# Kernel tuning notes

Hardware: AMD Instinct MI355X
Metric: run time of the kernel (lower is better)

Reference implementation:

```python
import jax, jax.numpy as jnp
import numpy as np

T, B, E, H = 2048, 2, 2048, 16
HD = E // H
SCALE = HD ** -0.5
NEG = -1e9  # large-negative additive mask (finite, safe in fp32/bf16)


def setup_inputs() -> dict:
    key = jax.random.key(0)
    ks = jax.random.split(key, 6)
    query = jax.random.normal(ks[0], (T, B, E), dtype=jnp.float32)
    # causal additive mask, as metaseq builds for decoder self-attention
    attn_mask = jnp.where(jnp.tril(jnp.ones((T, T), dtype=bool)), 0.0, NEG).astype(jnp.float32)
    # combined qkv projection: rows ordered [K | V | Q] per split_tensor_along_last_dim
    qkv_w = jax.random.normal(ks[1], (3 * E, E), dtype=jnp.float32) * (1.0 / np.sqrt(2 * E))
    qkv_b = jax.random.uniform(ks[2], (3 * E,), dtype=jnp.float32, minval=-1, maxval=1) / np.sqrt(E)
    out_w = jax.random.normal(ks[3], (E, E), dtype=jnp.float32) * (1.0 / np.sqrt(2 * E))
    out_b = jax.random.uniform(ks[4], (E,), dtype=jnp.float32, minval=-1, maxval=1) / np.sqrt(E)
    return {"query": query, "attn_mask": attn_mask, "qkv_w": qkv_w,
            "qkv_b": qkv_b, "out_w": out_w, "out_b": out_b}


def reference(query, attn_mask, qkv_w, qkv_b, out_w, out_b):
    t, b, e = query.shape
    # fused QKV projection (ColumnParallelLinear, world_size=1)
    kvq = jnp.einsum('tbe,fe->tbf', query, qkv_w) + qkv_b  # [T,B,3E]
    k, v, q = kvq[..., :e], kvq[..., e:2 * e], kvq[..., 2 * e:]
    q = q * SCALE
    q = q.reshape(t, b, H, HD)
    k = k.reshape(t, b, H, HD)
    v = v.reshape(t, b, H, HD)
    # explicit QK^T bmm -> [B,H,T,S]
    scores = jnp.einsum('tbhd,sbhd->bhts', q, k) + attn_mask[None, None]
    probs = jax.nn.softmax(scores, axis=-1)  # dropout p=0 -> identity
    ctx = jnp.einsum('bhts,sbhd->tbhd', probs, v).reshape(t, b, e)
    # RowParallelLinear out_proj (skip_bias_add in the original; bias added here)
    out = jnp.einsum('tbe,fe->tbf', ctx, out_w) + out_b
    return out
```

## Files before the change

### kernel.cpp

```cpp
#include <hip/hip_runtime.h>
#include <hip/hip_bf16.h>
#include <stdint.h>

#define T_DIM 2048
#define B_DIM 2
#define E_DIM 2048
#define H_DIM 16
#define HD_DIM 128
#define F_DIM 6144
#define ROWS 4096
#define KVB 64

#define QK_SCALE 0.08838834764831845f
#define LOG2E    1.4426950408889634f
#define RESCALE_THR 8.0f

typedef __bf16 bf16_t;
typedef __bf16 bf16x8 __attribute__((ext_vector_type(8)));
typedef __bf16 bf16x4 __attribute__((ext_vector_type(4)));
typedef float  f32x4  __attribute__((ext_vector_type(4)));

__device__ __forceinline__ void gll16(const void* g, void* l) {
  __builtin_amdgcn_global_load_lds((const __attribute__((address_space(1))) void*)g,
                                   (__attribute__((address_space(3))) void*)l, 16, 0, 0);
}

__global__ void cvt_f32_bf16(const float* __restrict__ src, bf16_t* __restrict__ dst, int n4) {
  int i = blockIdx.x * blockDim.x + threadIdx.x;
  int stride = gridDim.x * blockDim.x;
  for (; i < n4; i += stride) {
    float4 v = ((const float4*)src)[i];
    bf16x4 o;
    o[0] = (bf16_t)v.x; o[1] = (bf16_t)v.y; o[2] = (bf16_t)v.z; o[3] = (bf16_t)v.w;
    ((bf16x4*)dst)[i] = o;
  }
}

template<int EPI>
__launch_bounds__(256, 2)
__global__ void gemm_bt(const bf16_t* __restrict__ A, const bf16_t* __restrict__ Bm,
                        const float* __restrict__ bias, void* __restrict__ Cout,
                        int N, int K, int nbn, float qscale, int qcol0)
{
  __shared__ __align__(16) bf16_t As[128][64];
  __shared__ __align__(16) bf16_t Bs[128][64];

  int bid = blockIdx.x;
  int nwg = gridDim.x;
  int cpx = nwg >> 3;
  int swz = (bid & 7) * cpx + (bid >> 3);
  int bm = swz / nbn, bn = swz % nbn;

  int tid = threadIdx.x;
  int lane = tid & 63, wid = tid >> 6;
  int lr = lane & 15, lg = lane >> 4;
  int wm = wid >> 1, wn = wid & 1;

  f32x4 acc[4][4] = {};

  int srow8 = tid >> 3;
  int schunk = tid & 7;

  const bf16_t* gA = A + (size_t)(bm * 128) * K;
  const bf16_t* gB = Bm + (size_t)(bn * 128) * K;

  for (int k0 = 0; k0 < K; k0 += 64) {
    #pragma unroll
    for (int i = 0; i < 4; ++i) {
      int row = i * 32 + srow8;
      int sc = schunk ^ (row & 7);
      gll16(gA + (size_t)row * K + k0 + sc * 8, &As[row][schunk * 8]);
    }
    #pragma unroll
    for (int i = 0; i < 4; ++i) {
      int row = i * 32 + srow8;
      int sc = schunk ^ (row & 7);
      gll16(gB + (size_t)row * K + k0 + sc * 8, &Bs[row][schunk * 8]);
    }
    __syncthreads();

    #pragma unroll
    for (int kk = 0; kk < 2; ++kk) {
      bf16x8 af[4], bfr[4];
      #pragma unroll
      for (int mi = 0; mi < 4; ++mi) {
        int row = wm * 64 + mi * 16 + lr;
        int ch = (kk * 4 + lg) ^ (row & 7);
        af[mi] = *(const bf16x8*)&As[row][ch * 8];
      }
      #pragma unroll
      for (int ni = 0; ni < 4; ++ni) {
        int row = wn * 64 + ni * 16 + lr;
        int ch = (kk * 4 + lg) ^ (row & 7);
        bfr[ni] = *(const bf16x8*)&Bs[row][ch * 8];
      }
      #pragma unroll
      for (int mi = 0; mi < 4; ++mi)
        #pragma unroll
        for (int ni = 0; ni < 4; ++ni)
          acc[mi][ni] = __builtin_amdgcn_mfma_f32_16x16x32_bf16(af[mi], bfr[ni], acc[mi][ni], 0, 0, 0);
    }
    __syncthreads();
  }

  #pragma unroll
  for (int mi = 0; mi < 4; ++mi) {
    int row0 = bm * 128 + wm * 64 + mi * 16 + lg * 4;
    #pragma unroll
    for (int ni = 0; ni < 4; ++ni) {
      int col = bn * 128 + wn * 64 + ni * 16 + lr;
      float bv = bias[col];
      float scl = (EPI == 0 && col >= qcol0) ? qscale : 1.0f;
      #pragma unroll
      for (int r = 0; r < 4; ++r) {
        float v = (acc[mi][ni][r] + bv) * scl;
        if (EPI == 0) ((bf16_t*)Cout)[(size_t)(row0 + r) * N + col] = (bf16_t)v;
        else          ((float*)Cout)[(size_t)(row0 + r) * N + col] = v;
      }
    }
  }
}

__global__ void repack_vt(const bf16_t* __restrict__ KVQ, bf16_t* __restrict__ VTg)
{
  __shared__ __align__(16) bf16_t tile[64][136];
  int bid = blockIdx.x;
  int st = bid & 31, bh = bid >> 5;
  int b = bh >> 4, h = bh & 15;
  int s0 = st * 64;
  int tid = threadIdx.x;

  const bf16_t* vbase = KVQ + (size_t)b * F_DIM + E_DIM + (size_t)h * HD_DIM;
  #pragma unroll
  for (int i = 0; i < 4; ++i) {
    int row = i * 16 + (tid >> 4), c = tid & 15;
    bf16x8 v = *(const bf16x8*)(vbase + (size_t)(s0 + row) * B_DIM * F_DIM + c * 8);
    *(bf16x8*)&tile[row][c * 8] = v;
  }
  __syncthreads();
  bf16_t* out = VTg + (size_t)bh * HD_DIM * T_DIM;
  #pragma unroll
  for (int i = 0; i < 4; ++i) {
    int d = i * 32 + (tid >> 3), c = tid & 7;
    bf16x8 o;
    #pragma unroll
    for (int j = 0; j < 8; ++j) o[j] = tile[c * 8 + j][d];
    *(bf16x8*)(out + (size_t)d * T_DIM + s0 + c * 8) = o;
  }
}

__launch_bounds__(256, 2)
__global__ void attn3(const bf16_t* __restrict__ KVQ, const bf16_t* __restrict__ VTg,
                      bf16_t* __restrict__ CTX)
{
  __shared__ __align__(16) bf16_t Ks[2][KVB][128];
  __shared__ __align__(16) bf16_t Vs[2][128][KVB];
  __shared__ __align__(16) bf16_t Ps[4][32 * 64];

  int bid = blockIdx.x;
  int xcd = bid & 7;
  int j   = bid >> 3;
  int hi  = j >> 5;
  int mid = (j >> 4) & 1;
  int q   = j & 15;
  int bh  = xcd * 4 + hi * 2 + mid;
  int qt  = hi ? (15 - q) : q;
  int b = bh >> 4, h = bh & 15;

  int tid = threadIdx.x;
  int lane = tid & 63, wid = tid >> 6;
  int lr = lane & 15, lg = lane >> 4;

  const bf16_t* kbase = KVQ + (size_t)b * F_DIM + (size_t)h * HD_DIM;
  const bf16_t* vtb   = VTg + (size_t)bh * HD_DIM * T_DIM;
  bf16_t* PsW = &Ps[wid][0];

  bf16x8 qf[2][4];
  #pragma unroll
  for (int mf = 0; mf < 2; ++mf) {
    int t = qt * 128 + wid * 32 + mf * 16 + lr;
    const bf16_t* qb = KVQ + ((size_t)t * B_DIM + b) * F_DIM + 2 * E_DIM + h * HD_DIM;
    #pragma unroll
    for (int ks = 0; ks < 4; ++ks) qf[mf][ks] = *(const bf16x8*)(qb + ks * 32 + lg * 8);
  }

  f32x4 ctxa[2][8] = {};
  float m[2][4], lsum[2][4];
  #pragma unroll
  for (int mf = 0; mf < 2; ++mf)
    #pragma unroll
    for (int r = 0; r < 4; ++r) { m[mf][r] = -1e30f; lsum[mf][r] = 0.0f; }

  int krow = tid >> 4, kch = tid & 15;
  int vrow = tid >> 3, vch = tid & 7;

  auto stage = [&](int buf, int it) {
    int s0 = it * KVB;
    #pragma unroll
    for (int i = 0; i < 4; ++i) {
      int row = i * 16 + krow;
      int sc = kch ^ (row & 7);
      gll16(kbase + (size_t)(s0 + row) * B_DIM * F_DIM + sc * 8, &Ks[buf][row][kch * 8]);
    }
    #pragma unroll
    for (int i = 0; i < 4; ++i) {
      int row = i * 32 + vrow;
      int sc = vch ^ (row & 7);
      gll16(vtb + (size_t)row * T_DIM + s0 + sc * 8, &Vs[buf][row][vch * 8]);
    }
  };

  int nt = 2 * (qt + 1);
  stage(0, 0);
  __syncthreads();

  int tqw = qt * 128 + wid * 32;

  for (int it = 0; it < nt; ++it) {
    int cur = it & 1;
    if (it + 1 < nt) stage(cur ^ 1, it + 1);
    int s0 = it * KVB;
    bool diag = (it >= nt - 2);

    f32x4 sacc[2][4] = {};
    __builtin_amdgcn_s_setprio(1);
    #pragma unroll
    for (int ks = 0; ks < 4; ++ks) {
      #pragma unroll
      for (int nti = 0; nti < 4; ++nti) {
        int srow = nti * 16 + lr;
        int slot = (ks * 4 + lg) ^ (srow & 7);
        bf16x8 kf = *(const bf16x8*)&Ks[cur][srow][slot * 8];
        sacc[0][nti] = __builtin_amdgcn_mfma_f32_16x16x32_bf16(qf[0][ks], kf, sacc[0][nti], 0, 0, 0);
        sacc[1][nti] = __builtin_amdgcn_mfma_f32_16x16x32_bf16(qf[1][ks], kf, sacc[1][nti], 0, 0, 0);
      }
    }
    __builtin_amdgcn_s_setprio(0);

    float mxl = -1e30f;
    #pragma unroll
    for (int mf = 0; mf < 2; ++mf)
      #pragma unroll
      for (int r = 0; r < 4; ++r)
        #pragma unroll
        for (int nti = 0; nti < 4; ++nti) {
          float v = sacc[mf][nti][r];
          if (diag) v = (s0 + nti * 16 + lr > tqw + mf * 16 + lg * 4 + r) ? -1e30f : v;
          sacc[mf][nti][r] = v;
          mxl = fmaxf(mxl, v - m[mf][r]);
        }
    if (!__all(mxl <= RESCALE_THR)) {
      #pragma unroll
      for (int mf = 0; mf < 2; ++mf)
        #pragma unroll
        for (int r = 0; r < 4; ++r) {
          float mx = fmaxf(fmaxf(sacc[mf][0][r], sacc[mf][1][r]),
                           fmaxf(sacc[mf][2][r], sacc[mf][3][r]));
          #pragma unroll
          for (int d = 1; d < 16; d <<= 1) mx = fmaxf(mx, __shfl_xor(mx, d, 64));
          float mn = fmaxf(m[mf][r], mx);
          float rs = exp2f(m[mf][r] - mn);
          m[mf][r] = mn;
          lsum[mf][r] *= rs;
          #pragma unroll
          for (int dt = 0; dt < 8; ++dt) ctxa[mf][dt][r] *= rs;
        }
    }
    #pragma unroll
    for (int mf = 0; mf < 2; ++mf)
      #pragma unroll
      for (int r = 0; r < 4; ++r) {
        int prow = mf * 16 + lg * 4 + r;
        #pragma unroll
        for (int nti = 0; nti < 4; ++nti) {
          float p = exp2f(sacc[mf][nti][r] - m[mf][r]);
          lsum[mf][r] += p;
          int chk = (nti * 2 + (lr >> 3)) ^ (prow & 7);
          PsW[prow * 64 + chk * 8 + (lr & 7)] = (bf16_t)p;
        }
      }
    asm volatile("s_waitcnt lgkmcnt(0)" ::: "memory");
    __builtin_amdgcn_sched_barrier(0);

    bf16x8 pf[2][2];
    #pragma unroll
    for (int mf = 0; mf < 2; ++mf) {
      int prow = mf * 16 + lr;
      #pragma unroll
      for (int kh = 0; kh < 2; ++kh) {
        int chk = (kh * 4 + lg) ^ (prow & 7);
        pf[mf][kh] = *(const bf16x8*)&PsW[prow * 64 + chk * 8];
      }
    }
    __builtin_amdgcn_s_setprio(1);
    #pragma unroll
    for (int dt = 0; dt < 8; ++dt) {
      int drow = dt * 16 + lr;
      int sl0 = lg ^ (drow & 7);
      int sl1 = (4 + lg) ^ (drow & 7);
      bf16x8 vf0 = *(const bf16x8*)&Vs[cur][drow][sl0 * 8];
      bf16x8 vf1 = *(const bf16x8*)&Vs[cur][drow][sl1 * 8];
      ctxa[0][dt] = __builtin_amdgcn_mfma_f32_16x16x32_bf16(pf[0][0], vf0, ctxa[0][dt], 0, 0, 0);
      ctxa[0][dt] = __builtin_amdgcn_mfma_f32_16x16x32_bf16(pf[0][1], vf1, ctxa[0][dt], 0, 0, 0);
      ctxa[1][dt] = __builtin_amdgcn_mfma_f32_16x16x32_bf16(pf[1][0], vf0, ctxa[1][dt], 0, 0, 0);
      ctxa[1][dt] = __builtin_amdgcn_mfma_f32_16x16x32_bf16(pf[1][1], vf1, ctxa[1][dt], 0, 0, 0);
    }
    __builtin_amdgcn_s_setprio(0);

    __syncthreads();
  }

  #pragma unroll
  for (int mf = 0; mf < 2; ++mf)
    #pragma unroll
    for (int r = 0; r < 4; ++r) {
      #pragma unroll
      for (int d = 1; d < 16; d <<= 1) lsum[mf][r] += __shfl_xor(lsum[mf][r], d, 64);
    }

  #pragma unroll
  for (int mf = 0; mf < 2; ++mf)
    #pragma unroll
    for (int r = 0; r < 4; ++r) {
      int t = qt * 128 + wid * 32 + mf * 16 + lg * 4 + r;
      float inv = 1.0f / lsum[mf][r];
      bf16_t* out = CTX + ((size_t)t * B_DIM + b) * E_DIM + h * HD_DIM;
      #pragma unroll
      for (int dt = 0; dt < 8; ++dt)
        out[dt * 16 + lr] = (bf16_t)(ctxa[mf][dt][r] * inv);
    }
}

extern "C" void kernel_launch(void* const* d_in, const int* in_sizes, int n_in,
                              void* d_out, int out_size, void* d_ws, size_t ws_size,
                              hipStream_t stream)
{
  const float* query = (const float*)d_in[0];
  const float* qkv_w = (const float*)d_in[2];
  const float* qkv_b = (const float*)d_in[3];
  const float* out_w = (const float*)d_in[4];
  const float* out_b = (const float*)d_in[5];

  bf16_t* Xbf  = (bf16_t*)d_ws;
  bf16_t* Wqkv = Xbf  + (size_t)ROWS * E_DIM;
  bf16_t* Wout = Wqkv + (size_t)F_DIM * E_DIM;
  bf16_t* KVQ  = Wout + (size_t)E_DIM * E_DIM;
  bf16_t* CTX  = Xbf;
  bf16_t* VTg  = Wqkv;

  cvt_f32_bf16<<<2048, 256, 0, stream>>>(query, Xbf,  ROWS * E_DIM / 4);
  cvt_f32_bf16<<<2048, 256, 0, stream>>>(qkv_w, Wqkv, F_DIM * E_DIM / 4);
  cvt_f32_bf16<<<2048, 256, 0, stream>>>(out_w, Wout, E_DIM * E_DIM / 4);

  gemm_bt<0><<<32 * 48, 256, 0, stream>>>(Xbf, Wqkv, qkv_b, KVQ,
                                          F_DIM, E_DIM, 48, QK_SCALE * LOG2E, 2 * E_DIM);

  repack_vt<<<32 * 32, 256, 0, stream>>>(KVQ, VTg);

  attn3<<<512, 256, 0, stream>>>(KVQ, VTg, CTX);

  gemm_bt<1><<<32 * 16, 256, 0, stream>>>(CTX, Wout, out_b, (float*)d_out,
                                          E_DIM, E_DIM, 16, 1.0f, 1 << 30);
}
```

Before: 281.7 us.

## Triple-buffer GEMM LDS loads with 128x256 tiles and 512-thread blocks

Replaces the single-buffered 128x128 GEMM with a 512-thread kernel that computes 128x256 tiles and prefetches two K-steps ahead into a three-slot LDS ring using direct global-to-LDS loads. Explicit vmcnt waits and raw barriers replace the per-step syncthreads. All fragments are preloaded before the MFMA burst, which runs at raised wave priority. The aim is to hide global load latency and raise operand reuse. The cost is much more LDS per block (~144KB), which may limit occupancy to one block per CU, plus fewer blocks for the output projection (256).

```diff
diff --git a/kernel.cpp b/kernel.cpp
--- a/kernel.cpp
+++ b/kernel.cpp
@@ -37,70 +37,96 @@
 }
 
 template<int EPI>
-__launch_bounds__(256, 2)
-__global__ void gemm_bt(const bf16_t* __restrict__ A, const bf16_t* __restrict__ Bm,
+__launch_bounds__(512, 2)
+__global__ void gemm_dp(const bf16_t* __restrict__ A, const bf16_t* __restrict__ Bm,
                         const float* __restrict__ bias, void* __restrict__ Cout,
                         int N, int K, int nbn, float qscale, int qcol0)
 {
-  __shared__ __align__(16) bf16_t As[128][64];
-  __shared__ __align__(16) bf16_t Bs[128][64];
+  __shared__ __align__(16) bf16_t As[3][128][64];
+  __shared__ __align__(16) bf16_t Bs[3][256][64];
 
   int bid = blockIdx.x;
-  int nwg = gridDim.x;
-  int cpx = nwg >> 3;
+  int cpx = gridDim.x >> 3;
   int swz = (bid & 7) * cpx + (bid >> 3);
   int bm = swz / nbn, bn = swz % nbn;
 
   int tid = threadIdx.x;
   int lane = tid & 63, wid = tid >> 6;
   int lr = lane & 15, lg = lane >> 4;
-  int wm = wid >> 1, wn = wid & 1;
+  int wm = wid >> 2, wn = wid & 3;
 
   f32x4 acc[4][4] = {};
 
-  int srow8 = tid >> 3;
+  int srow = tid >> 3;
   int schunk = tid & 7;
 
   const bf16_t* gA = A + (size_t)(bm * 128) * K;
-  const bf16_t* gB = Bm + (size_t)(bn * 128) * K;
-
-  for (int k0 = 0; k0 < K; k0 += 64) {
+  const bf16_t* gB = Bm + (size_t)(bn * 256) * K;
+
+  int nt = K >> 6;
+
+  auto stage = [&](int kt, int slot) {
+    int k0 = kt * 64;
+    #pragma unroll
+    for (int i = 0; i < 2; ++i) {
+      int row = i * 64 + srow;
+      int sc = schunk ^ (row & 7);
+      gll16(gA + (size_t)row * K + k0 + sc * 8, &As[slot][row][schunk * 8]);
+    }
     #pragma unroll
     for (int i = 0; i < 4; ++i) {
-      int row = i * 32 + srow8;
+      int row = i * 64 + srow;
       int sc = schunk ^ (row & 7);
-      gll16(gA + (size_t)row * K + k0 + sc * 8, &As[row][schunk * 8]);
-    }
-    #pragma unroll
-    for (int i = 0; i < 4; ++i) {
-      int row = i * 32 + srow8;
-      int sc = schunk ^ (row & 7);
-      gll16(gB + (size_t)row * K + k0 + sc * 8, &Bs[row][schunk * 8]);
-    }
-    __syncthreads();
-
+      gll16(gB + (size_t)row * K + k0 + sc * 8, &Bs[slot][row][schunk * 8]);
+    }
+  };
+
+  stage(0, 0);
+  if (nt > 1) stage(1, 1);
+
+  for (int t = 0; t < nt; ++t) {
+    int slot = t % 3;
+    if (t + 2 < nt) {
+      stage(t + 2, (t + 2) % 3);
+      asm volatile("s_waitcnt vmcnt(12)" ::: "memory");
+    } else if (t + 2 == nt) {
+      asm volatile("s_waitcnt vmcnt(6)" ::: "memory");
+    } else {
+      asm volatile("s_waitcnt vmcnt(0)" ::: "memory");
+    }
+    __builtin_amdgcn_sched_barrier(0);
+    __builtin_amdgcn_s_barrier();
+    __builtin_amdgcn_sched_barrier(0);
+
+    bf16x8 af[2][4], bfm[2][4];
     #pragma unroll
     for (int kk = 0; kk < 2; ++kk) {
-      bf16x8 af[4], bfr[4];
       #pragma unroll
       for (int mi = 0; mi < 4; ++mi) {
         int row = wm * 64 + mi * 16 + lr;
         int ch = (kk * 4 + lg) ^ (row & 7);
-        af[mi] = *(const bf16x8*)&As[row][ch * 8];
+        af[kk][mi] = *(const bf16x8*)&As[slot][row][ch * 8];
       }
       #pragma unroll
       for (int ni = 0; ni < 4; ++ni) {
         int row = wn * 64 + ni * 16 + lr;
         int ch = (kk * 4 + lg) ^ (row & 7);
-        bfr[ni] = *(const bf16x8*)&Bs[row][ch * 8];
-      }
+        bfm[kk][ni] = *(const bf16x8*)&Bs[slot][row][ch * 8];
+      }
+    }
+    __builtin_amdgcn_s_setprio(1);
+    #pragma unroll
+    for (int kk = 0; kk < 2; ++kk)
       #pragma unroll
       for (int mi = 0; mi < 4; ++mi)
         #pragma unroll
         for (int ni = 0; ni < 4; ++ni)
-          acc[mi][ni] = __builtin_amdgcn_mfma_f32_16x16x32_bf16(af[mi], bfr[ni], acc[mi][ni], 0, 0, 0);
-    }
-    __syncthreads();
+          acc[mi][ni] = __builtin_amdgcn_mfma_f32_16x16x32_bf16(af[kk][mi], bfm[kk][ni], acc[mi][ni], 0, 0, 0);
+    __builtin_amdgcn_s_setprio(0);
+
+    __builtin_amdgcn_sched_barrier(0);
+    __builtin_amdgcn_s_barrier();
+    __builtin_amdgcn_sched_barrier(0);
   }
 
   #pragma unroll
@@ -108,7 +134,7 @@
     int row0 = bm * 128 + wm * 64 + mi * 16 + lg * 4;
     #pragma unroll
     for (int ni = 0; ni < 4; ++ni) {
-      int col = bn * 128 + wn * 64 + ni * 16 + lr;
+      int col = bn * 256 + wn * 64 + ni * 16 + lr;
       float bv = bias[col];
       float scl = (EPI == 0 && col >= qcol0) ? qscale : 1.0f;
       #pragma unroll
@@ -352,13 +378,13 @@
   cvt_f32_bf16<<<2048, 256, 0, stream>>>(qkv_w, Wqkv, F_DIM * E_DIM / 4);
   cvt_f32_bf16<<<2048, 256, 0, stream>>>(out_w, Wout, E_DIM * E_DIM / 4);
 
-  gemm_bt<0><<<32 * 48, 256, 0, stream>>>(Xbf, Wqkv, qkv_b, KVQ,
-                                          F_DIM, E_DIM, 48, QK_SCALE * LOG2E, 2 * E_DIM);
+  gemm_dp<0><<<768, 512, 0, stream>>>(Xbf, Wqkv, qkv_b, KVQ,
+                                      F_DIM, E_DIM, 24, QK_SCALE * LOG2E, 2 * E_DIM);
 
   repack_vt<<<32 * 32, 256, 0, stream>>>(KVQ, VTg);
 
   attn3<<<512, 256, 0, stream>>>(KVQ, VTg, CTX);
 
-  gemm_bt<1><<<32 * 16, 256, 0, stream>>>(CTX, Wout, out_b, (float*)d_out,
-                                          E_DIM, E_DIM, 16, 1.0f, 1 << 30);
-}
+  gemm_dp<1><<<256, 512, 0, stream>>>(CTX, Wout, out_b, (float*)d_out,
+                                      E_DIM, E_DIM, 8, 1.0f, 1 << 30);
+}
```

Measured after the change: 308.3 us. 1.09x slower.

## Use 256x256-tile double-buffered GEMM with 8 waves for QKV projection

Applied to the files above, without the earlier changes.

Replaces the 128x128-tile QKV projection GEMM with a new 512-thread kernel that computes 256x256 output tiles. It double-buffers 64-wide K slices in LDS, loaded asynchronously with XOR swizzling, and splits each iteration's MFMA work into two halves so the next stage's loads start mid-iteration. Raising MFMA priority during compute aims to keep the matrix units busy. The larger tile improves data reuse and cuts global traffic, but it uses 128 KB of LDS per block and yields only 384 blocks, which may reduce occupancy and leave part of the GPU idle at the tail.

```diff
diff --git a/kernel.cpp b/kernel.cpp
--- a/kernel.cpp
+++ b/kernel.cpp
@@ -119,6 +119,134 @@
       }
     }
   }
+}
+
+template<int EPI>
+__launch_bounds__(512, 2)
+__global__ void gemm_dp2(const bf16_t* __restrict__ A, const bf16_t* __restrict__ Bm,
+                         const float* __restrict__ bias, void* __restrict__ Cout,
+                         int N, int K, int nbn, float qscale, int qcol0)
+{
+  __shared__ __align__(16) bf16_t As[2][256][64];
+  __shared__ __align__(16) bf16_t Bs[2][256][64];
+
+  int bid = blockIdx.x;
+  int cpx = gridDim.x >> 3;
+  int swz = (bid & 7) * cpx + (bid >> 3);
+  int bm = swz / nbn, bn = swz % nbn;
+
+  int tid = threadIdx.x;
+  int lane = tid & 63, wid = tid >> 6;
+  int lr = lane & 15, lg = lane >> 4;
+  int wm = wid >> 2, wn = wid & 3;
+
+  f32x4 acc[8][4] = {};
+
+  int srow = tid >> 3;
+  int schunk = tid & 7;
+
+  const bf16_t* gA = A + (size_t)(bm * 256) * K;
+  const bf16_t* gB = Bm + (size_t)(bn * 256) * K;
+
+  int nt = K >> 6;
+
+  auto stage = [&](int kt, int buf) {
+    int k0 = kt * 64;
+    #pragma unroll
+    for (int i = 0; i < 4; ++i) {
+      int row = i * 64 + srow;
+      int sc = schunk ^ (row & 7);
+      gll16(gA + (size_t)row * K + k0 + sc * 8, &As[buf][row][schunk * 8]);
+    }
+    #pragma unroll
+    for (int i = 0; i < 4; ++i) {
+      int row = i * 64 + srow;
+      int sc = schunk ^ (row & 7);
+      gll16(gB + (size_t)row * K + k0 + sc * 8, &Bs[buf][row][schunk * 8]);
+    }
+  };
+
+  stage(0, 0);
+  if (nt > 1) stage(1, 1);
+  asm volatile("s_waitcnt vmcnt(8)" ::: "memory");
+  asm volatile("s_barrier" ::: "memory");
+
+  for (int t = 0; t < nt; ++t) {
+    int buf = t & 1;
+
+    bf16x8 a0[4][2], bfr[4][2];
+    #pragma unroll
+    for (int mi = 0; mi < 4; ++mi)
+      #pragma unroll
+      for (int kk = 0; kk < 2; ++kk) {
+        int row = wm * 128 + mi * 16 + lr;
+        int ch = (kk * 4 + lg) ^ (row & 7);
+        a0[mi][kk] = *(const bf16x8*)&As[buf][row][ch * 8];
+      }
+    #pragma unroll
+    for (int ni = 0; ni < 4; ++ni)
+      #pragma unroll
+      for (int kk = 0; kk < 2; ++kk) {
+        int row = wn * 64 + ni * 16 + lr;
+        int ch = (kk * 4 + lg) ^ (row & 7);
+        bfr[ni][kk] = *(const bf16x8*)&Bs[buf][row][ch * 8];
+      }
+    __builtin_amdgcn_s_setprio(1);
+    #pragma unroll
+    for (int kk = 0; kk < 2; ++kk)
+      #pragma unroll
+      for (int mi = 0; mi < 4; ++mi)
+        #pragma unroll
+        for (int ni = 0; ni < 4; ++ni)
+          acc[mi][ni] = __builtin_amdgcn_mfma_f32_16x16x32_bf16(a0[mi][kk], bfr[ni][kk], acc[mi][ni], 0, 0, 0);
+    __builtin_amdgcn_s_setprio(0);
+
+    bf16x8 a1[4][2];
+    #pragma unroll
+    for (int mi = 0; mi < 4; ++mi)
+      #pragma unroll
+      for (int kk = 0; kk < 2; ++kk) {
+        int row = wm * 128 + 64 + mi * 16 + lr;
+        int ch = (kk * 4 + lg) ^ (row & 7);
+        a1[mi][kk] = *(const bf16x8*)&As[buf][row][ch * 8];
+      }
+    asm volatile("s_waitcnt lgkmcnt(0)" ::: "memory");
+    asm volatile("s_barrier" ::: "memory");
+    if (t + 2 < nt) stage(t + 2, buf);
+
+    __builtin_amdgcn_s_setprio(1);
+    #pragma unroll
+    for (int kk = 0; kk < 2; ++kk)
+      #pragma unroll
+      for (int mi = 0; mi < 4; ++mi)
+        #pragma unroll
+        for (int ni = 0; ni < 4; ++ni)
+          acc[4 + mi][ni] = __builtin_amdgcn_mfma_f32_16x16x32_bf16(a1[mi][kk], bfr[ni][kk], acc[4 + mi][ni], 0, 0, 0);
+    __builtin_amdgcn_s_setprio(0);
+
+    if (t + 2 < nt)      asm volatile("s_waitcnt vmcnt(8)" ::: "memory");
+    else if (t + 1 < nt) asm volatile("s_waitcnt vmcnt(0)" ::: "memory");
+    asm volatile("s_barrier" ::: "memory");
+  }
+
+  #pragma unroll
+  for (int qm = 0; qm < 2; ++qm)
+    #pragma unroll
+    for (int mi = 0; mi < 4; ++mi) {
+      int row0 = bm * 256 + wm * 128 + qm * 64 + mi * 16 + lg * 4;
+      #pragma unroll
+      for (int ni = 0; ni < 4; ++ni) {
+        int col = bn * 256 + wn * 64 + ni * 16 + lr;
+        float bv = bias[col];
+        float scl = (EPI == 0 && col >= qcol0) ? qscale : 1.0f;
+        #pragma unroll
+        for (int r = 0; r < 4; ++r) {
+          float v = (acc[qm * 4 + mi][ni][r] + bv) * scl;
+          if (EPI == 0) ((bf16_t*)Cout)[(size_t)(row0 + r) * N + col] = (bf16_t)v;
+          else          ((float*)Cout)[(size_t)(row0 + r) * N + col] = v;
+        }
+      }
+    }
 }
 
 __global__ void repack_vt(const bf16_t* __restrict__ KVQ, bf16_t* __restrict__ VTg)
@@ -352,8 +480,8 @@
   cvt_f32_bf16<<<2048, 256, 0, stream>>>(qkv_w, Wqkv, F_DIM * E_DIM / 4);
   cvt_f32_bf16<<<2048, 256, 0, stream>>>(out_w, Wout, E_DIM * E_DIM / 4);
 
-  gemm_bt<0><<<32 * 48, 256, 0, stream>>>(Xbf, Wqkv, qkv_b, KVQ,
-                                          F_DIM, E_DIM, 48, QK_SCALE * LOG2E, 2 * E_DIM);
+  gemm_dp2<0><<<384, 512, 0, stream>>>(Xbf, Wqkv, qkv_b, KVQ,
+                                       F_DIM, E_DIM, 24, QK_SCALE * LOG2E, 2 * E_DIM);
 
   repack_vt<<<32 * 32, 256, 0, stream>>>(KVQ, VTg);
 
```

Measured after the change: 272.5 us. 1.03x faster.

## Use 256x256-tile 8-wave ping-pong GEMM for QKV projection

Applied to the files above, without the earlier changes.

Adds a new GEMM kernel with 256x256 output tiles, 512 threads (8 waves), double-buffered LDS filled by direct global-to-LDS loads, and a four-phase schedule that interleaves quadrant MFMAs with prefetches under barriers and raised wave priority. It replaces the 128x128 QKV projection launch to raise arithmetic intensity and overlap loads with compute. The cost is a large LDS footprint (128KB), heavy register use, and only 384 blocks, which may limit occupancy and leave a wave-quantization tail. The out-projection still uses the old kernel.

```diff
diff --git a/kernel.cpp b/kernel.cpp
--- a/kernel.cpp
+++ b/kernel.cpp
@@ -119,6 +119,149 @@
       }
     }
   }
+}
+
+template<int EPI>
+__launch_bounds__(512, 2)
+__global__ void gemm_8p(const bf16_t* __restrict__ A, const bf16_t* __restrict__ Bm,
+                        const float* __restrict__ bias, void* __restrict__ Cout,
+                        int N, int K, int nbn, float qscale, int qcol0)
+{
+  __shared__ __align__(16) bf16_t As[2][2][128][64];
+  __shared__ __align__(16) bf16_t Bs[2][2][128][64];
+
+  int bid = blockIdx.x;
+  int cpx = gridDim.x >> 3;
+  int swz = (bid & 7) * cpx + (bid >> 3);
+  int bm = swz / nbn, bn = swz % nbn;
+
+  int tid = threadIdx.x;
+  int lane = tid & 63, wid = tid >> 6;
+  int lr = lane & 15, lg = lane >> 4;
+  int vm = wid >> 2, vn = wid & 3;
+
+  int srow = tid >> 3, schunk = tid & 7;
+
+  const bf16_t* gA = A + (size_t)(bm * 256) * K;
+  const bf16_t* gB = Bm + (size_t)(bn * 256) * K;
+  int nt = K >> 6;
+
+  f32x4 acc[2][2][4][2] = {};
+
+  auto stA = [&](int kt, int buf, int h) {
+    int k0 = kt * 64;
+    #pragma unroll
+    for (int i = 0; i < 2; ++i) {
+      int row = i * 64 + srow;
+      int sc = schunk ^ (row & 7);
+      gll16(gA + (size_t)(h * 128 + row) * K + k0 + sc * 8, &As[buf][h][row][schunk * 8]);
+    }
+  };
+  auto stB = [&](int kt, int buf, int h) {
+    int k0 = kt * 64;
+    #pragma unroll
+    for (int i = 0; i < 2; ++i) {
+      int row = i * 64 + srow;
+      int sc = schunk ^ (row & 7);
+      gll16(gB + (size_t)(h * 128 + row) * K + k0 + sc * 8, &Bs[buf][h][row][schunk * 8]);
+    }
+  };
+
+  bf16x8 af[4][2];
+  bf16x8 bfr[2][2][2];
+
+#define LOAD_A(QM)                                                              \
+  _Pragma("unroll")                                                             \
+  for (int mi = 0; mi < 4; ++mi) {                                              \
+    int row = vm * 64 + mi * 16 + lr;                                           \
+    _Pragma("unroll")                                                           \
+    for (int kk = 0; kk < 2; ++kk)                                              \
+      af[mi][kk] = *(const bf16x8*)&As[buf][QM][row][((kk * 4 + lg) ^ (row & 7)) * 8]; \
+  }
+#define LOAD_B(QN)                                                              \
+  _Pragma("unroll")                                                             \
+  for (int ni = 0; ni < 2; ++ni) {                                              \
+    int row = vn * 32 + ni * 16 + lr;                                           \
+    _Pragma("unroll")                                                           \
+    for (int kk = 0; kk < 2; ++kk)                                              \
+      bfr[QN][ni][kk] = *(const bf16x8*)&Bs[buf][QN][row][((kk * 4 + lg) ^ (row & 7)) * 8]; \
+  }
+#define MFMA_Q(QM, QN)                                                          \
+  __builtin_amdgcn_s_setprio(1);                                                \
+  _Pragma("unroll")                                                             \
+  for (int kk = 0; kk < 2; ++kk)                                                \
+    _Pragma("unroll")                                                           \
+    for (int mi = 0; mi < 4; ++mi)                                              \
+      _Pragma("unroll")                                                         \
+      for (int ni = 0; ni < 2; ++ni)                                            \
+        acc[QM][QN][mi][ni] = __builtin_amdgcn_mfma_f32_16x16x32_bf16(          \
+            af[mi][kk], bfr[QN][ni][kk], acc[QM][QN][mi][ni], 0, 0, 0);         \
+  __builtin_amdgcn_s_setprio(0);
+
+  stA(0, 0, 0); stB(0, 0, 1); stA(0, 0, 1); stB(0, 0, 0);
+  if (nt > 1) { stA(1, 1, 0); stB(1, 1, 1); }
+  asm volatile("s_waitcnt vmcnt(4)" ::: "memory");
+  __builtin_amdgcn_s_barrier();
+
+  for (int t = 0; t < nt; ++t) {
+    int buf = t & 1;
+
+    LOAD_A(0)
+    LOAD_B(0)
+    if (t + 1 < nt) stA(t + 1, buf ^ 1, 1);
+    __builtin_amdgcn_s_barrier();
+    asm volatile("s_waitcnt lgkmcnt(0)" ::: "memory");
+    MFMA_Q(0, 0)
+    __builtin_amdgcn_s_barrier();
+
+    LOAD_B(1)
+    if (t + 1 < nt) stB(t + 1, buf ^ 1, 0);
+    __builtin_amdgcn_s_barrier();
+    asm volatile("s_waitcnt lgkmcnt(0)" ::: "memory");
+    MFMA_Q(0, 1)
+    __builtin_amdgcn_s_barrier();
+
+    LOAD_A(1)
+    if (t + 2 < nt) stA(t + 2, buf, 0);
+    __builtin_amdgcn_s_barrier();
+    asm volatile("s_waitcnt lgkmcnt(0)" ::: "memory");
+    MFMA_Q(1, 1)
+    __builtin_amdgcn_s_barrier();
+
+    if (t + 2 < nt) {
+      stB(t + 2, buf, 1);
+      asm volatile("s_waitcnt vmcnt(4)" ::: "memory");
+    } else {
+      asm volatile("s_waitcnt vmcnt(0)" ::: "memory");
+    }
+    __builtin_amdgcn_s_barrier();
+    MFMA_Q(1, 0)
+    __builtin_amdgcn_s_barrier();
+  }
+#undef LOAD_A
+#undef LOAD_B
+#undef MFMA_Q
+
+  #pragma unroll
+  for (int qm = 0; qm < 2; ++qm)
+    #pragma unroll
+    for (int qn = 0; qn < 2; ++qn)
+      #pragma unroll
+      for (int mi = 0; mi < 4; ++mi) {
+        int row0 = bm * 256 + qm * 128 + vm * 64 + mi * 16 + lg * 4;
+        #pragma unroll
+        for (int ni = 0; ni < 2; ++ni) {
+          int col = bn * 256 + qn * 128 + vn * 32 + ni * 16 + lr;
+          float bv = bias[col];
+          float scl = (EPI == 0 && col >= qcol0) ? qscale : 1.0f;
+          #pragma unroll
+          for (int r = 0; r < 4; ++r) {
+            float v = (acc[qm][qn][mi][ni][r] + bv) * scl;
+            if (EPI == 0) ((bf16_t*)Cout)[(size_t)(row0 + r) * N + col] = (bf16_t)v;
+            else          ((float*)Cout)[(size_t)(row0 + r) * N + col] = v;
+          }
+        }
+      }
 }
 
 __global__ void repack_vt(const bf16_t* __restrict__ KVQ, bf16_t* __restrict__ VTg)
@@ -352,8 +495,8 @@
   cvt_f32_bf16<<<2048, 256, 0, stream>>>(qkv_w, Wqkv, F_DIM * E_DIM / 4);
   cvt_f32_bf16<<<2048, 256, 0, stream>>>(out_w, Wout, E_DIM * E_DIM / 4);
 
-  gemm_bt<0><<<32 * 48, 256, 0, stream>>>(Xbf, Wqkv, qkv_b, KVQ,
-                                          F_DIM, E_DIM, 48, QK_SCALE * LOG2E, 2 * E_DIM);
+  gemm_8p<0><<<384, 512, 0, stream>>>(Xbf, Wqkv, qkv_b, KVQ,
+                                      F_DIM, E_DIM, 24, QK_SCALE * LOG2E, 2 * E_DIM);
 
   repack_vt<<<32 * 32, 256, 0, stream>>>(KVQ, VTg);
 
```

Result: no change. 276.7 us (-1.8%).
